# Optimization experiments

Hardware: AMD Instinct MI355X
Metric: run time of the kernel (lower is better)

The kernel has to match this reference:

```python
import jax, jax.numpy as jnp
import numpy as np

B, N, IN, HID, OUT = 32768, 16, 64, 128, 128

def setup_inputs() -> dict:
    key = jax.random.key(0)
    ks = jax.random.split(key, 8)
    x = jax.random.normal(ks[0], (B * N, IN), dtype=jnp.float32)
    edge_index0 = jax.random.randint(ks[1], (B * 8,), 0, B * N, dtype=jnp.int64)
    adj_param = jnp.ones((N, N), dtype=jnp.float32)
    s1 = 1.0 / np.sqrt(IN)
    s2 = 1.0 / np.sqrt(HID)
    W_rel1 = jax.random.normal(ks[2], (IN, HID), dtype=jnp.float32) * s1
    b_rel1 = jax.random.normal(ks[3], (HID,), dtype=jnp.float32) * s1
    W_root1 = jax.random.normal(ks[4], (IN, HID), dtype=jnp.float32) * s1
    W_rel2 = jax.random.normal(ks[5], (HID, OUT), dtype=jnp.float32) * s2
    b_rel2 = jax.random.normal(ks[6], (OUT,), dtype=jnp.float32) * s2
    W_root2 = jax.random.normal(ks[7], (HID, OUT), dtype=jnp.float32) * s2
    return {"x": x, "edge_index0": edge_index0, "adj_param": adj_param,
            "W_rel1": W_rel1, "b_rel1": b_rel1, "W_root1": W_root1,
            "W_rel2": W_rel2, "b_rel2": b_rel2, "W_root2": W_root2}

def _dense_sage(x, adj, W_rel, b_rel, W_root):
    # DenseSAGEConv: mean-aggregate neighbors via dense adj, then lin_rel + lin_root
    agg = jnp.einsum('bij,bjf->bif', adj, x)                     # [B,N,F]
    deg = jnp.maximum(adj.sum(-1, keepdims=True), 1.0)           # clamp(min=1)
    return (agg / deg) @ W_rel + b_rel + x @ W_root

def reference(x, edge_index0, adj_param, W_rel1, b_rel1, W_root1, W_rel2, b_rel2, W_root2):
    b = x.shape[0] // N
    xb = x.reshape(b, N, -1)
    # nodes touched by an edge keep adjacency; others masked out (rows and cols zeroed)
    mask = jnp.ones((b * N,), dtype=bool).at[edge_index0].set(False).reshape(b, N)
    drop = mask[:, :, None] | mask[:, None, :]                   # [B,N,N]
    adj = jnp.where(drop, 0.0, adj_param[None, :, :])
    h = jax.nn.relu(_dense_sage(xb, adj, W_rel1, b_rel1, W_root1))
    out = _dense_sage(h, adj, W_rel2, b_rel2, W_root2)
    return out.reshape(b * N, -1)
```

## Files before the change

### kernel.cpp

```cpp
#include <hip/hip_runtime.h>

typedef unsigned short u16;
typedef float floatx4 __attribute__((ext_vector_type(4)));
typedef short shortx8 __attribute__((ext_vector_type(8)));

#define MFMA16(a, b, c) __builtin_amdgcn_mfma_f32_16x16x32_bf16(a, b, c, 0, 0, 0)

__device__ __forceinline__ u16 f2b(float f) {
    union { float f; unsigned u; } c;
    c.f = f;
    unsigned lsb = (c.u >> 16) & 1u;
    c.u += 0x7fffu + lsb;
    return (u16)(c.u >> 16);
}

__global__ __launch_bounds__(256) void scatter_flags(const int* __restrict__ e,
                                                     unsigned char* __restrict__ fl,
                                                     int n) {
    int i = blockIdx.x * 256 + threadIdx.x;
    if (i < n) fl[e[i]] = 1;
}

__global__ __launch_bounds__(256) void prep_weights(
    const float* __restrict__ W1r, const float* __restrict__ W1o,
    const float* __restrict__ W2r, const float* __restrict__ W2o,
    u16* __restrict__ W1rt, u16* __restrict__ W1ot,
    u16* __restrict__ W2rt, u16* __restrict__ W2ot)
{
    int t = blockIdx.x * 256 + threadIdx.x;
    union { u16 h[4]; unsigned long long ll; } pk;
    if (t < 2048) {
        int n = t >> 4, k0 = (t & 15) * 4;
        #pragma unroll
        for (int j = 0; j < 4; ++j) pk.h[j] = f2b(W1r[(k0 + j) * 128 + n]);
        *(unsigned long long*)(W1rt + n * 64 + k0) = pk.ll;
    } else if (t < 4096) {
        int tt = t - 2048; int n = tt >> 4, k0 = (tt & 15) * 4;
        #pragma unroll
        for (int j = 0; j < 4; ++j) pk.h[j] = f2b(W1o[(k0 + j) * 128 + n]);
        *(unsigned long long*)(W1ot + n * 64 + k0) = pk.ll;
    } else if (t < 8192) {
        int tt = t - 4096; int n = tt >> 5, k0 = (tt & 31) * 4;
        #pragma unroll
        for (int j = 0; j < 4; ++j) pk.h[j] = f2b(W2r[(k0 + j) * 128 + n]);
        *(unsigned long long*)(W2rt + n * 128 + k0) = pk.ll;
    } else if (t < 12288) {
        int tt = t - 8192; int n = tt >> 5, k0 = (tt & 31) * 4;
        #pragma unroll
        for (int j = 0; j < 4; ++j) pk.h[j] = f2b(W2o[(k0 + j) * 128 + n]);
        *(unsigned long long*)(W2ot + n * 128 + k0) = pk.ll;
    }
}

__global__ __launch_bounds__(256, 5) void sage_mfma(
    const float* __restrict__ x,
    const unsigned char* __restrict__ flags,
    const float* __restrict__ adjp,
    const float* __restrict__ br1,
    const float* __restrict__ br2,
    const u16* __restrict__ W1rt,
    const u16* __restrict__ W1ot,
    const u16* __restrict__ W2rt,
    const u16* __restrict__ W2ot,
    float* __restrict__ out)
{
    __shared__ __align__(16) unsigned char smem[27904];
    u16*   s_x   = (u16*)smem;
    u16*   s_h   = (u16*)(smem + 9216);
    float* s_adj = (float*)(smem + 26624);
    float* s_flag= (float*)(smem + 27648);

    const int b   = blockIdx.x;
    const int tid = threadIdx.x;
    const int w   = tid >> 6;
    const int l   = tid & 63;
    const int q   = l >> 4;
    const int lr  = l & 15;
    const int tn0 = 2 * w;
    const floatx4 fz = {0.f, 0.f, 0.f, 0.f};

    {
        const float4* xg = (const float4*)(x + (size_t)b * 4096);
        #pragma unroll
        for (int i = 0; i < 4; ++i) {
            int e = tid + i * 256;
            float4 v = xg[e];
            int row = e >> 4, f = (e & 15) * 4;
            union { u16 h[4]; unsigned long long ll; } pk;
            pk.h[0] = f2b(v.x); pk.h[1] = f2b(v.y); pk.h[2] = f2b(v.z); pk.h[3] = f2b(v.w);
            *(unsigned long long*)(s_x + row * 72 + f) = pk.ll;
        }
    }
    if (tid < 64) s_flag[tid] = flags[b * 64 + tid] ? 1.0f : 0.0f;
    s_adj[tid] = adjp[tid];
    __syncthreads();

    shortx8 wb8[4];
    #pragma unroll
    for (int g = 0; g < 4; ++g) {
        float s = 0.f;
        #pragma unroll
        for (int j = 0; j < 16; ++j) s += s_adj[lr * 16 + j] * s_flag[g * 16 + j];
        float fi = s_flag[g * 16 + lr];
        float ti = fi / fmaxf(s * fi, 1.0f);
        #pragma unroll
        for (int jj = 0; jj < 4; ++jj) {
            int j = q * 4 + jj;
            wb8[g][jj] = (short)f2b(ti * s_flag[g * 16 + j] * s_adj[lr * 16 + j]);
            wb8[g][jj + 4] = 0;
        }
    }

    shortx8 b1r[2][2], b1o[2][2];
    floatx4 bias1[2], bias2[2];
    #pragma unroll
    for (int tni = 0; tni < 2; ++tni) {
        int n0 = (tn0 + tni) * 16;
        bias1[tni] = *(const floatx4*)(br1 + n0 + q * 4);
        bias2[tni] = *(const floatx4*)(br2 + n0 + q * 4);
        int n = n0 + lr;
        #pragma unroll
        for (int ks = 0; ks < 2; ++ks) {
            b1r[tni][ks] = *(const shortx8*)(W1rt + n * 64 + ks * 32 + q * 8);
            b1o[tni][ks] = *(const shortx8*)(W1ot + n * 64 + ks * 32 + q * 8);
        }
    }

    #pragma unroll
    for (int tm = 0; tm < 4; ++tm) {
        shortx8 ax[2];
        #pragma unroll
        for (int ks = 0; ks < 2; ++ks)
            ax[ks] = *(const shortx8*)(s_x + (tm * 16 + lr) * 72 + ks * 32 + q * 8);
        #pragma unroll
        for (int tni = 0; tni < 2; ++tni) {
            floatx4 y1 = fz, y2t = bias1[tni];
            #pragma unroll
            for (int ks = 0; ks < 2; ++ks) {
                y1  = MFMA16(ax[ks], b1r[tni][ks], y1);
                y2t = MFMA16(b1o[tni][ks], ax[ks], y2t);
            }
            shortx8 a1 = {(short)f2b(y1[0]), (short)f2b(y1[1]),
                          (short)f2b(y1[2]), (short)f2b(y1[3]), 0, 0, 0, 0};
            floatx4 ag = MFMA16(a1, wb8[tm], y2t);
            union { u16 h[4]; unsigned long long ll; } pk;
            #pragma unroll
            for (int r = 0; r < 4; ++r) pk.h[r] = f2b(fmaxf(ag[r], 0.f));
            *(unsigned long long*)(s_h + (tm * 16 + lr) * 136 +
                                   (tn0 + tni) * 16 + q * 4) = pk.ll;
        }
    }
    __syncthreads();

    #pragma unroll
    for (int tni = 0; tni < 2; ++tni) {
        int n = (tn0 + tni) * 16 + lr;
        shortx8 b2r[4], b2o[4];
        #pragma unroll
        for (int ks = 0; ks < 4; ++ks) {
            b2r[ks] = *(const shortx8*)(W2rt + n * 128 + ks * 32 + q * 8);
            b2o[ks] = *(const shortx8*)(W2ot + n * 128 + ks * 32 + q * 8);
        }
        #pragma unroll
        for (int tm = 0; tm < 4; ++tm) {
            floatx4 u1 = fz, u2t = bias2[tni];
            #pragma unroll
            for (int ks = 0; ks < 4; ++ks) {
                shortx8 ah = *(const shortx8*)(s_h + (tm * 16 + lr) * 136 +
                                               ks * 32 + q * 8);
                u1  = MFMA16(ah, b2r[ks], u1);
                u2t = MFMA16(b2o[ks], ah, u2t);
            }
            shortx8 a2 = {(short)f2b(u1[0]), (short)f2b(u1[1]),
                          (short)f2b(u1[2]), (short)f2b(u1[3]), 0, 0, 0, 0};
            floatx4 og = MFMA16(a2, wb8[tm], u2t);
            *(floatx4*)(out + ((size_t)b * 64 + tm * 16 + lr) * 128 +
                        (tn0 + tni) * 16 + q * 4) = og;
        }
    }
}

extern "C" void kernel_launch(void* const* d_in, const int* in_sizes, int n_in,
                              void* d_out, int out_size, void* d_ws, size_t ws_size,
                              hipStream_t stream) {
    const float* x    = (const float*)d_in[0];
    const int*   edge = (const int*)d_in[1];
    const float* adjp = (const float*)d_in[2];
    const float* W1r  = (const float*)d_in[3];
    const float* br1  = (const float*)d_in[4];
    const float* W1o  = (const float*)d_in[5];
    const float* W2r  = (const float*)d_in[6];
    const float* br2  = (const float*)d_in[7];
    const float* W2o  = (const float*)d_in[8];
    float* out = (float*)d_out;

    const int total_nodes = in_sizes[0] / 64;
    const int nedge       = in_sizes[1];
    const int nblocks     = total_nodes / 64;

    unsigned char* flags = (unsigned char*)d_ws;
    u16* wbase = (u16*)((char*)d_ws + 524288);
    u16* W1rt = wbase;
    u16* W1ot = wbase + 8192;
    u16* W2rt = wbase + 16384;
    u16* W2ot = wbase + 32768;

    hipMemsetAsync(flags, 0, (size_t)total_nodes, stream);
    scatter_flags<<<(nedge + 255) / 256, 256, 0, stream>>>(edge, flags, nedge);
    prep_weights<<<48, 256, 0, stream>>>(W1r, W1o, W2r, W2o, W1rt, W1ot, W2rt, W2ot);
    sage_mfma<<<nblocks, 256, 0, stream>>>(x, flags, adjp, br1, br2,
                                           W1rt, W1ot, W2rt, W2ot, out);
}
```

Before: 458.6 us.

## Assign one graph per wavefront and drop block-level shared staging and barriers

Restructures the fused SAGE kernel so each wavefront owns one 16-node graph and computes all 128 output columns, instead of four waves splitting columns across four graphs per block. x is loaded straight from global into MFMA operand registers, the degree and normalized adjacency are computed with shuffles from packed flag words, and the only shared memory left is a per-wave h buffer, so both __syncthreads calls go away. Weights are now streamed from global/L2 inside the column loops rather than held in registers, which adds weight-load traffic per wave. Occupancy hint raised from 5 to 6 blocks.

```diff
diff --git a/kernel.cpp b/kernel.cpp
--- a/kernel.cpp
+++ b/kernel.cpp
@@ -12,6 +12,15 @@
     unsigned lsb = (c.u >> 16) & 1u;
     c.u += 0x7fffu + lsb;
     return (u16)(c.u >> 16);
+}
+
+__device__ __forceinline__ shortx8 pack8(float4 a, float4 b) {
+    shortx8 r;
+    r[0] = (short)f2b(a.x); r[1] = (short)f2b(a.y);
+    r[2] = (short)f2b(a.z); r[3] = (short)f2b(a.w);
+    r[4] = (short)f2b(b.x); r[5] = (short)f2b(b.y);
+    r[6] = (short)f2b(b.z); r[7] = (short)f2b(b.w);
+    return r;
 }
 
 __global__ __launch_bounds__(256) void scatter_flags(const int* __restrict__ e,
@@ -52,7 +61,7 @@
     }
 }
 
-__global__ __launch_bounds__(256, 5) void sage_mfma(
+__global__ __launch_bounds__(256, 6) void sage_mfma(
     const float* __restrict__ x,
     const unsigned char* __restrict__ flags,
     const float* __restrict__ adjp,
@@ -64,119 +73,92 @@
     const u16* __restrict__ W2ot,
     float* __restrict__ out)
 {
-    __shared__ __align__(16) unsigned char smem[27904];
-    u16*   s_x   = (u16*)smem;
-    u16*   s_h   = (u16*)(smem + 9216);
-    float* s_adj = (float*)(smem + 26624);
-    float* s_flag= (float*)(smem + 27648);
+    __shared__ __align__(16) u16 smem[4 * 2176];
 
-    const int b   = blockIdx.x;
     const int tid = threadIdx.x;
     const int w   = tid >> 6;
     const int l   = tid & 63;
     const int q   = l >> 4;
     const int lr  = l & 15;
-    const int tn0 = 2 * w;
+    const int gg  = blockIdx.x * 4 + w;
+    u16* hrow = smem + w * 2176;
     const floatx4 fz = {0.f, 0.f, 0.f, 0.f};
 
-    {
-        const float4* xg = (const float4*)(x + (size_t)b * 4096);
+    const float* xrow = x + ((size_t)gg * 16 + lr) * 64 + q * 8;
+    float4 xv0 = *(const float4*)(xrow);
+    float4 xv1 = *(const float4*)(xrow + 4);
+    float4 xv2 = *(const float4*)(xrow + 32);
+    float4 xv3 = *(const float4*)(xrow + 36);
+
+    const uint4  flv = *(const uint4*)(flags + (size_t)gg * 16);
+    const float4 av  = *(const float4*)(adjp + lr * 16 + q * 4);
+
+    unsigned wq = (q == 0) ? flv.x : (q == 1) ? flv.y : (q == 2) ? flv.z : flv.w;
+    float fj0 = (float)((wq      ) & 1u);
+    float fj1 = (float)((wq >>  8) & 1u);
+    float fj2 = (float)((wq >> 16) & 1u);
+    float fj3 = (float)((wq >> 24) & 1u);
+    float p = av.x * fj0 + av.y * fj1 + av.z * fj2 + av.w * fj3;
+    p += __shfl_xor(p, 16);
+    p += __shfl_xor(p, 32);
+    int lw = lr >> 2;
+    unsigned wl = (lw == 0) ? flv.x : (lw == 1) ? flv.y : (lw == 2) ? flv.z : flv.w;
+    float fi = (float)((wl >> ((lr & 3) * 8)) & 1u);
+    float ti = fi / fmaxf(p * fi, 1.0f);
+    shortx8 wb8 = {0, 0, 0, 0, 0, 0, 0, 0};
+    wb8[0] = (short)f2b(ti * fj0 * av.x);
+    wb8[1] = (short)f2b(ti * fj1 * av.y);
+    wb8[2] = (short)f2b(ti * fj2 * av.z);
+    wb8[3] = (short)f2b(ti * fj3 * av.w);
+
+    shortx8 ax[2];
+    ax[0] = pack8(xv0, xv1);
+    ax[1] = pack8(xv2, xv3);
+
+    #pragma unroll
+    for (int tni = 0; tni < 8; ++tni) {
+        const u16* w1p = W1rt + (tni * 16 + lr) * 64 + q * 8;
+        const u16* w1q = W1ot + (tni * 16 + lr) * 64 + q * 8;
+        shortx8 b1r0 = *(const shortx8*)(w1p);
+        shortx8 b1r1 = *(const shortx8*)(w1p + 32);
+        shortx8 b1o0 = *(const shortx8*)(w1q);
+        shortx8 b1o1 = *(const shortx8*)(w1q + 32);
+        floatx4 bias1 = *(const floatx4*)(br1 + tni * 16 + q * 4);
+        floatx4 y1 = MFMA16(ax[0], b1r0, fz);
+        y1 = MFMA16(ax[1], b1r1, y1);
+        floatx4 y2t = MFMA16(b1o0, ax[0], bias1);
+        y2t = MFMA16(b1o1, ax[1], y2t);
+        shortx8 a1 = {(short)f2b(y1[0]), (short)f2b(y1[1]),
+                      (short)f2b(y1[2]), (short)f2b(y1[3]), 0, 0, 0, 0};
+        floatx4 ag = MFMA16(a1, wb8, y2t);
+        union { u16 h[4]; unsigned long long ll; } pk;
         #pragma unroll
-        for (int i = 0; i < 4; ++i) {
-            int e = tid + i * 256;
-            float4 v = xg[e];
-            int row = e >> 4, f = (e & 15) * 4;
-            union { u16 h[4]; unsigned long long ll; } pk;
-            pk.h[0] = f2b(v.x); pk.h[1] = f2b(v.y); pk.h[2] = f2b(v.z); pk.h[3] = f2b(v.w);
-            *(unsigned long long*)(s_x + row * 72 + f) = pk.ll;
-        }
-    }
-    if (tid < 64) s_flag[tid] = flags[b * 64 + tid] ? 1.0f : 0.0f;
-    s_adj[tid] = adjp[tid];
-    __syncthreads();
-
-    shortx8 wb8[4];
-    #pragma unroll
-    for (int g = 0; g < 4; ++g) {
-        float s = 0.f;
-        #pragma unroll
-        for (int j = 0; j < 16; ++j) s += s_adj[lr * 16 + j] * s_flag[g * 16 + j];
-        float fi = s_flag[g * 16 + lr];
-        float ti = fi / fmaxf(s * fi, 1.0f);
-        #pragma unroll
-        for (int jj = 0; jj < 4; ++jj) {
-            int j = q * 4 + jj;
-            wb8[g][jj] = (short)f2b(ti * s_flag[g * 16 + j] * s_adj[lr * 16 + j]);
-            wb8[g][jj + 4] = 0;
-        }
+        for (int r = 0; r < 4; ++r) pk.h[r] = f2b(fmaxf(ag[r], 0.f));
+        *(unsigned long long*)(hrow + lr * 136 + tni * 16 + q * 4) = pk.ll;
     }
 
-    shortx8 b1r[2][2], b1o[2][2];
-    floatx4 bias1[2], bias2[2];
+    shortx8 ah[4];
     #pragma unroll
-    for (int tni = 0; tni < 2; ++tni) {
-        int n0 = (tn0 + tni) * 16;
-        bias1[tni] = *(const floatx4*)(br1 + n0 + q * 4);
-        bias2[tni] = *(const floatx4*)(br2 + n0 + q * 4);
-        int n = n0 + lr;
-        #pragma unroll
-        for (int ks = 0; ks < 2; ++ks) {
-            b1r[tni][ks] = *(const shortx8*)(W1rt + n * 64 + ks * 32 + q * 8);
-            b1o[tni][ks] = *(const shortx8*)(W1ot + n * 64 + ks * 32 + q * 8);
-        }
-    }
+    for (int ks = 0; ks < 4; ++ks)
+        ah[ks] = *(const shortx8*)(hrow + lr * 136 + ks * 32 + q * 8);
 
     #pragma unroll
-    for (int tm = 0; tm < 4; ++tm) {
-        shortx8 ax[2];
-        #pragma unroll
-        for (int ks = 0; ks < 2; ++ks)
-            ax[ks] = *(const shortx8*)(s_x + (tm * 16 + lr) * 72 + ks * 32 + q * 8);
-        #pragma unroll
-        for (int tni = 0; tni < 2; ++tni) {
-            floatx4 y1 = fz, y2t = bias1[tni];
-            #pragma unroll
-            for (int ks = 0; ks < 2; ++ks) {
-                y1  = MFMA16(ax[ks], b1r[tni][ks], y1);
-                y2t = MFMA16(b1o[tni][ks], ax[ks], y2t);
-            }
-            shortx8 a1 = {(short)f2b(y1[0]), (short)f2b(y1[1]),
-                          (short)f2b(y1[2]), (short)f2b(y1[3]), 0, 0, 0, 0};
-            floatx4 ag = MFMA16(a1, wb8[tm], y2t);
-            union { u16 h[4]; unsigned long long ll; } pk;
-            #pragma unroll
-            for (int r = 0; r < 4; ++r) pk.h[r] = f2b(fmaxf(ag[r], 0.f));
-            *(unsigned long long*)(s_h + (tm * 16 + lr) * 136 +
-                                   (tn0 + tni) * 16 + q * 4) = pk.ll;
-        }
-    }
-    __syncthreads();
-
-    #pragma unroll
-    for (int tni = 0; tni < 2; ++tni) {
-        int n = (tn0 + tni) * 16 + lr;
-        shortx8 b2r[4], b2o[4];
+    for (int tni = 0; tni < 8; ++tni) {
+        const u16* w2p = W2rt + (tni * 16 + lr) * 128 + q * 8;
+        const u16* w2q = W2ot + (tni * 16 + lr) * 128 + q * 8;
+        floatx4 u1 = fz;
+        floatx4 u2t = *(const floatx4*)(br2 + tni * 16 + q * 4);
         #pragma unroll
         for (int ks = 0; ks < 4; ++ks) {
-            b2r[ks] = *(const shortx8*)(W2rt + n * 128 + ks * 32 + q * 8);
-            b2o[ks] = *(const shortx8*)(W2ot + n * 128 + ks * 32 + q * 8);
+            shortx8 br_ = *(const shortx8*)(w2p + ks * 32);
+            shortx8 bo_ = *(const shortx8*)(w2q + ks * 32);
+            u1  = MFMA16(ah[ks], br_, u1);
+            u2t = MFMA16(bo_, ah[ks], u2t);
         }
-        #pragma unroll
-        for (int tm = 0; tm < 4; ++tm) {
-            floatx4 u1 = fz, u2t = bias2[tni];
-            #pragma unroll
-            for (int ks = 0; ks < 4; ++ks) {
-                shortx8 ah = *(const shortx8*)(s_h + (tm * 16 + lr) * 136 +
-                                               ks * 32 + q * 8);
-                u1  = MFMA16(ah, b2r[ks], u1);
-                u2t = MFMA16(b2o[ks], ah, u2t);
-            }
-            shortx8 a2 = {(short)f2b(u1[0]), (short)f2b(u1[1]),
-                          (short)f2b(u1[2]), (short)f2b(u1[3]), 0, 0, 0, 0};
-            floatx4 og = MFMA16(a2, wb8[tm], u2t);
-            *(floatx4*)(out + ((size_t)b * 64 + tm * 16 + lr) * 128 +
-                        (tn0 + tni) * 16 + q * 4) = og;
-        }
+        shortx8 a2 = {(short)f2b(u1[0]), (short)f2b(u1[1]),
+                      (short)f2b(u1[2]), (short)f2b(u1[3]), 0, 0, 0, 0};
+        floatx4 og = MFMA16(a2, wb8, u2t);
+        *(floatx4*)(out + ((size_t)gg * 16 + lr) * 128 + tni * 16 + q * 4) = og;
     }
 }
 
```

Result: slower. 679.5 us (+48.2%).

## Compute adjacency weights in registers with shuffles, drop LDS staging and buffer output stores

Applied to the files above, without the earlier changes.

Flags and the adjacency parameter are now read straight into registers, and the per-row degree sums are reduced with wave shuffles instead of staging through shared memory. This removes one LDS round trip and lets the x-tile conversion overlap with the weight computation, since only one barrier remains before layer one. Final outputs are buffered in registers and written after all MFMAs, so the two 16-column tiles of each row are stored back to back. Occupancy bounds are lowered to 4 blocks per SIMD to make room for the extra live registers, which may reduce latency hiding.

```diff
diff --git a/kernel.cpp b/kernel.cpp
--- a/kernel.cpp
+++ b/kernel.cpp
@@ -52,7 +52,7 @@
     }
 }
 
-__global__ __launch_bounds__(256, 5) void sage_mfma(
+__global__ __launch_bounds__(256, 4) void sage_mfma(
     const float* __restrict__ x,
     const unsigned char* __restrict__ flags,
     const float* __restrict__ adjp,
@@ -64,11 +64,9 @@
     const u16* __restrict__ W2ot,
     float* __restrict__ out)
 {
-    __shared__ __align__(16) unsigned char smem[27904];
-    u16*   s_x   = (u16*)smem;
-    u16*   s_h   = (u16*)(smem + 9216);
-    float* s_adj = (float*)(smem + 26624);
-    float* s_flag= (float*)(smem + 27648);
+    __shared__ __align__(16) unsigned char smem[26624];
+    u16* s_x = (u16*)smem;
+    u16* s_h = (u16*)(smem + 9216);
 
     const int b   = blockIdx.x;
     const int tid = threadIdx.x;
@@ -79,6 +77,12 @@
     const int tn0 = 2 * w;
     const floatx4 fz = {0.f, 0.f, 0.f, 0.f};
 
+    uint4 flv[4];
+    #pragma unroll
+    for (int g = 0; g < 4; ++g)
+        flv[g] = *(const uint4*)(flags + (size_t)b * 64 + g * 16);
+    const float4 av = *(const float4*)(adjp + lr * 16 + q * 4);
+
     {
         const float4* xg = (const float4*)(x + (size_t)b * 4096);
         #pragma unroll
@@ -91,24 +95,30 @@
             *(unsigned long long*)(s_x + row * 72 + f) = pk.ll;
         }
     }
-    if (tid < 64) s_flag[tid] = flags[b * 64 + tid] ? 1.0f : 0.0f;
-    s_adj[tid] = adjp[tid];
-    __syncthreads();
 
     shortx8 wb8[4];
     #pragma unroll
     for (int g = 0; g < 4; ++g) {
-        float s = 0.f;
-        #pragma unroll
-        for (int j = 0; j < 16; ++j) s += s_adj[lr * 16 + j] * s_flag[g * 16 + j];
-        float fi = s_flag[g * 16 + lr];
-        float ti = fi / fmaxf(s * fi, 1.0f);
-        #pragma unroll
-        for (int jj = 0; jj < 4; ++jj) {
-            int j = q * 4 + jj;
-            wb8[g][jj] = (short)f2b(ti * s_flag[g * 16 + j] * s_adj[lr * 16 + j]);
-            wb8[g][jj + 4] = 0;
-        }
+        unsigned wq = (q == 0) ? flv[g].x : (q == 1) ? flv[g].y
+                    : (q == 2) ? flv[g].z : flv[g].w;
+        float fj0 = (float)((wq      ) & 1u);
+        float fj1 = (float)((wq >>  8) & 1u);
+        float fj2 = (float)((wq >> 16) & 1u);
+        float fj3 = (float)((wq >> 24) & 1u);
+        float p = av.x * fj0 + av.y * fj1 + av.z * fj2 + av.w * fj3;
+        p += __shfl_xor(p, 16);
+        p += __shfl_xor(p, 32);
+        int lw = lr >> 2;
+        unsigned wl = (lw == 0) ? flv[g].x : (lw == 1) ? flv[g].y
+                    : (lw == 2) ? flv[g].z : flv[g].w;
+        float fi = (float)((wl >> ((lr & 3) * 8)) & 1u);
+        float ti = fi / fmaxf(p * fi, 1.0f);
+        shortx8 t = {0, 0, 0, 0, 0, 0, 0, 0};
+        t[0] = (short)f2b(ti * fj0 * av.x);
+        t[1] = (short)f2b(ti * fj1 * av.y);
+        t[2] = (short)f2b(ti * fj2 * av.z);
+        t[3] = (short)f2b(ti * fj3 * av.w);
+        wb8[g] = t;
     }
 
     shortx8 b1r[2][2], b1o[2][2];
@@ -125,6 +135,7 @@
             b1o[tni][ks] = *(const shortx8*)(W1ot + n * 64 + ks * 32 + q * 8);
         }
     }
+    __syncthreads();
 
     #pragma unroll
     for (int tm = 0; tm < 4; ++tm) {
@@ -152,6 +163,7 @@
     }
     __syncthreads();
 
+    floatx4 ogbuf[2][4];
     #pragma unroll
     for (int tni = 0; tni < 2; ++tni) {
         int n = (tn0 + tni) * 16 + lr;
@@ -173,10 +185,14 @@
             }
             shortx8 a2 = {(short)f2b(u1[0]), (short)f2b(u1[1]),
                           (short)f2b(u1[2]), (short)f2b(u1[3]), 0, 0, 0, 0};
-            floatx4 og = MFMA16(a2, wb8[tm], u2t);
-            *(floatx4*)(out + ((size_t)b * 64 + tm * 16 + lr) * 128 +
-                        (tn0 + tni) * 16 + q * 4) = og;
-        }
+            ogbuf[tni][tm] = MFMA16(a2, wb8[tm], u2t);
+        }
+    }
+    #pragma unroll
+    for (int tm = 0; tm < 4; ++tm) {
+        float* op = out + ((size_t)b * 64 + tm * 16 + lr) * 128 + tn0 * 16 + q * 4;
+        *(floatx4*)(op)      = ogbuf[0][tm];
+        *(floatx4*)(op + 16) = ogbuf[1][tm];
     }
 }
 
```

Result: faster. 446.4 us (-2.7%).
